# Performance work log

Measured on AMD Instinct MI355X. Metric: run time of the kernel, lower is better.

The kernel has to match this reference:

```python
import jax, jax.numpy as jnp
import numpy as np

BETA = 0.5

def gelu(x):
    return jax.nn.gelu(x, approximate=False)  # torch F.gelu default is exact erf

def setup_inputs() -> dict:
    key = jax.random.key(0)
    ks = jax.random.split(key, 10)
    N, F, PH, P, D, H, C, E = 50000, 128, 64, 8, 4, 128, 10, 1600000
    s = 0.05
    return {
        "x": jax.random.normal(ks[0], (N, F), jnp.float32),
        "W_proj": jax.random.normal(ks[1], (PH, F), jnp.float32) * s,
        "b_proj": jnp.zeros((PH,), jnp.float32),
        "W_x": jax.random.normal(ks[2], (H, F), jnp.float32) * s,
        "b_x": jnp.zeros((H,), jnp.float32),
        "W_path": jax.random.normal(ks[3], (H, D * PH), jnp.float32) * s,
        "b_path": jnp.zeros((H,), jnp.float32),
        "W_A": jax.random.normal(ks[4], (H, N), jnp.float32) * s,
        "b_A": jnp.zeros((H,), jnp.float32),
        "W_end": jax.random.normal(ks[5], (C, H), jnp.float32) * s,
        "b_end": jnp.zeros((C,), jnp.float32),
        "index": jax.random.randint(ks[6], (N, P, D), 0, N, jnp.int64)
                 if jax.config.jax_enable_x64 else jax.random.randint(ks[6], (N, P, D), 0, N, jnp.int32),
        "edge_index": jax.random.randint(ks[7], (2, E), 0, N, jnp.int32),
    }

def reference(x, W_proj, b_proj, W_x, b_x, W_path, b_path, W_A, b_A, W_end, b_end, index, edge_index):
    N = x.shape[0]
    # path projection then per-node path gather: [N, P, D, PH]
    pp = x @ W_proj.T + b_proj
    path = pp[index]
    Np, P, D, PH = path.shape
    # node MLP (dropout off in eval)
    h = gelu(x @ W_x.T + b_x)  # [N, H]
    # concat path encoder: [N, P, D*PH] -> [N, P, H]
    pi = gelu(path.reshape(Np, P, D * PH) @ W_path.T + b_path)
    # dot-product path attention with softmax over path dim
    att = jax.nn.softmax(jnp.einsum('nh,nph->np', h, pi), axis=-1)
    path_agg = jnp.einsum('np,nph->nh', att, pi)
    # sparse adjacency (COO, weights=1) times Linear weight: A @ W_A.T + b_A
    M = W_A.T  # [N, H]
    A_x = jax.ops.segment_sum(M[edge_index[1]], edge_index[0], num_segments=N) + b_A
    out = (1.0 - BETA) * (path_agg + h) + BETA * A_x
    out = gelu(out)
    return out @ W_end.T + b_end
```

## Files before the change

kernel.cpp:

```cpp
#include <hip/hip_runtime.h>
#include <hip/hip_bf16.h>
#include <math.h>

#define NF   128
#define NPH  64
#define NP   8
#define ND   4
#define NH   128
#define NC   10

typedef __bf16 bf16;
typedef __attribute__((ext_vector_type(4))) __bf16 bf16x4;
typedef __attribute__((ext_vector_type(8))) __bf16 bf16x8;
typedef __attribute__((ext_vector_type(4))) float f32x4;

__device__ __forceinline__ float gelu_fast(float x) {
    float z = fabsf(x) * 0.70710678118654752f;
    float t = 1.0f / (1.0f + 0.47047f * z);
    float poly = t * (0.3480242f + t * (-0.0958798f + t * 0.7478556f));
    float erfv = 1.0f - poly * __expf(-z * z);
    float s = copysignf(erfv, x);
    return 0.5f * x * (1.0f + s);
}

#define GLOAD_LDS16(g, l)                                                     \
    __builtin_amdgcn_global_load_lds(                                         \
        (const __attribute__((address_space(1))) unsigned int*)(g),           \
        (__attribute__((address_space(3))) unsigned int*)(l), 16, 0, 0)

__device__ __forceinline__ bf16x8 cvt8(float4 a, float4 b) {
    bf16x8 r;
    r[0] = (bf16)a.x; r[1] = (bf16)a.y; r[2] = (bf16)a.z; r[3] = (bf16)a.w;
    r[4] = (bf16)b.x; r[5] = (bf16)b.y; r[6] = (bf16)b.z; r[7] = (bf16)b.w;
    return r;
}

__global__ __launch_bounds__(256) void k_proj(
    const float* __restrict__ x,
    const float* __restrict__ Wproj, const float* __restrict__ bproj,
    const float* __restrict__ Wx,    const float* __restrict__ bx,
    bf16* __restrict__ pp, float* __restrict__ h, int N)
{
    __shared__ alignas(16) bf16 x_s[64 * 136];
    const int tid = threadIdx.x;
    const int w = tid >> 6, l = tid & 63;
    const int c = l & 15, g = l >> 4;

    bf16x8 bfr[3][4];
    float bias[3];
    #pragma unroll
    for (int t = 0; t < 3; ++t) {
        int ch = (w * 3 + t) * 16 + c;
        const float* wr = (ch < NPH) ? &Wproj[(size_t)ch * NF]
                                     : &Wx[(size_t)(ch - NPH) * NF];
        bias[t] = (ch < NPH) ? bproj[ch] : bx[ch - NPH];
        #pragma unroll
        for (int ks = 0; ks < 4; ++ks) {
            const float* src = wr + ks * 32 + g * 8;
            bfr[t][ks] = cvt8(*(const float4*)src, *(const float4*)(src + 4));
        }
    }

    const int n0 = blockIdx.x * 64;
    #pragma unroll
    for (int rr = 0; rr < 8; ++rr) {
        int id  = rr * 256 + tid;
        int row = id >> 5, c4 = id & 31;
        float4 v = make_float4(0.f, 0.f, 0.f, 0.f);
        if (n0 + row < N) v = *(const float4*)&x[(size_t)(n0 + row) * NF + c4 * 4];
        bf16x4 o;
        o[0] = (bf16)v.x; o[1] = (bf16)v.y; o[2] = (bf16)v.z; o[3] = (bf16)v.w;
        *(bf16x4*)&x_s[row * 136 + c4 * 4] = o;
    }
    __syncthreads();

    f32x4 acc[4][3] = {};
    #pragma unroll
    for (int rt = 0; rt < 4; ++rt)
        #pragma unroll
        for (int ks = 0; ks < 4; ++ks) {
            bf16x8 a = *(const bf16x8*)&x_s[(rt * 16 + c) * 136 + ks * 32 + g * 8];
            #pragma unroll
            for (int t = 0; t < 3; ++t)
                acc[rt][t] = __builtin_amdgcn_mfma_f32_16x16x32_bf16(
                    a, bfr[t][ks], acc[rt][t], 0, 0, 0);
        }

    #pragma unroll
    for (int rt = 0; rt < 4; ++rt) {
        #pragma unroll
        for (int t = 0; t < 3; ++t) {
            int ch = (w * 3 + t) * 16 + c;
            #pragma unroll
            for (int i = 0; i < 4; ++i) {
                int n = n0 + rt * 16 + g * 4 + i;
                if (n >= N) continue;
                float v = acc[rt][t][i] + bias[t];
                if (ch < NPH) pp[(size_t)n * NPH + ch] = (bf16)v;
                else          h[(size_t)n * NH + (ch - NPH)] = gelu_fast(v);
            }
        }
    }
}

__global__ __launch_bounds__(256) void k_path(
    const bf16* __restrict__ pp, const float* __restrict__ h,
    const float* __restrict__ Wpath, const float* __restrict__ bpath,
    const int* __restrict__ index, float* __restrict__ aggbuf,
    int N, int nrounds)
{
    __shared__ alignas(16) bf16 path_s[2][32 * 256];
    __shared__ alignas(16) float h_s[2][4][128];
    __shared__ float s_red[4][32];

    const int tid = threadIdx.x;
    const int w   = tid >> 6;
    const int l   = tid & 63;
    const int c   = l & 15;
    const int g   = l >> 4;
    const int nl  = g >> 1;
    const bool hi_half = (g & 1);

    bf16x8 bfrag[2][8];
    #pragma unroll
    for (int ht = 0; ht < 2; ++ht) {
        int hg = (w * 2 + ht) * 16 + c;
        #pragma unroll
        for (int ks = 0; ks < 8; ++ks) {
            const float* src = &Wpath[(size_t)hg * 256 + ks * 32 + g * 8];
            bfrag[ht][ks] = cvt8(*(const float4*)src, *(const float4*)(src + 4));
        }
    }
    const float bp0 = bpath[(w * 2 + 0) * 16 + c];
    const float bp1 = bpath[(w * 2 + 1) * 16 + c];

    auto stage = [&](int round, int b) {
        const int n0 = round * 4;
        #pragma unroll
        for (int rr = 0; rr < 4; ++rr) {
            int id  = rr * 256 + tid;
            int row = id >> 5;
            int cc  = id & 31;
            int ls  = cc ^ (row & 7);
            int d   = ls >> 3, q = ls & 7;
            int nn  = row >> 3, p = row & 7;
            int idx = index[(size_t)(n0 + nn) * (NP * ND) + p * ND + d];
            GLOAD_LDS16(pp + (size_t)idx * NPH + q * 8, &path_s[b][id * 8]);
        }
        if (tid < 128) {
            int node = tid >> 5, q = tid & 31;
            GLOAD_LDS16(&h[(size_t)(n0 + node) * NH + q * 4], &h_s[b][node][q * 4]);
        }
    };

    int r = blockIdx.x;
    const int G = gridDim.x;
    if (r < nrounds) stage(r, 0);
    int buf = 0;

    for (; r < nrounds; r += G) {
        const int n0 = r * 4;
        __syncthreads();
        if (r + G < nrounds) stage(r + G, buf ^ 1);

        f32x4 acc[2][2] = {};
        #pragma unroll
        for (int rt = 0; rt < 2; ++rt) {
            const int rowbase = (rt * 16 + c) * 256;
            #pragma unroll
            for (int ks = 0; ks < 8; ++ks) {
                int chunk = (ks * 4 + g) ^ (c & 7);
                bf16x8 a = *(const bf16x8*)&path_s[buf][rowbase + chunk * 8];
                acc[rt][0] = __builtin_amdgcn_mfma_f32_16x16x32_bf16(
                    a, bfrag[0][ks], acc[rt][0], 0, 0, 0);
                acc[rt][1] = __builtin_amdgcn_mfma_f32_16x16x32_bf16(
                    a, bfrag[1][ks], acc[rt][1], 0, 0, 0);
            }
        }

        float pi[2][2][4];
        #pragma unroll
        for (int rt = 0; rt < 2; ++rt) {
            const float hv0 = h_s[buf][rt * 2 + nl][w * 32 + c];
            const float hv1 = h_s[buf][rt * 2 + nl][w * 32 + 16 + c];
            float sp[4];
            #pragma unroll
            for (int i = 0; i < 4; ++i) {
                pi[rt][0][i] = gelu_fast(acc[rt][0][i] + bp0);
                pi[rt][1][i] = gelu_fast(acc[rt][1][i] + bp1);
                sp[i] = hv0 * pi[rt][0][i] + hv1 * pi[rt][1][i];
            }
            #pragma unroll
            for (int off = 1; off < 16; off <<= 1)
                #pragma unroll
                for (int i = 0; i < 4; ++i) sp[i] += __shfl_xor(sp[i], off, 64);
            float v = (c == 0) ? sp[0] : (c == 1) ? sp[1] : (c == 2) ? sp[2] : sp[3];
            if (c < 4) s_red[w][rt * 16 + g * 4 + c] = v;
        }

        __builtin_amdgcn_sched_barrier(0);
        asm volatile("s_waitcnt lgkmcnt(0)" ::: "memory");
        __builtin_amdgcn_s_barrier();
        __builtin_amdgcn_sched_barrier(0);

        #pragma unroll
        for (int rt = 0; rt < 2; ++rt) {
            float st[4];
            #pragma unroll
            for (int i = 0; i < 4; ++i) {
                int row = rt * 16 + g * 4 + i;
                st[i] = s_red[0][row] + s_red[1][row] +
                        s_red[2][row] + s_red[3][row];
            }
            float m4 = fmaxf(fmaxf(st[0], st[1]), fmaxf(st[2], st[3]));
            float m  = fmaxf(m4, __shfl_xor(m4, 16, 64));
            float e[4], s4 = 0.f;
            #pragma unroll
            for (int i = 0; i < 4; ++i) { e[i] = __expf(st[i] - m); s4 += e[i]; }
            float den = s4 + __shfl_xor(s4, 16, 64);
            const float inv = 1.0f / den;

            float pa0 = 0.f, pa1 = 0.f;
            #pragma unroll
            for (int i = 0; i < 4; ++i) {
                pa0 += e[i] * pi[rt][0][i];
                pa1 += e[i] * pi[rt][1][i];
            }
            pa0 = (pa0 + __shfl_xor(pa0, 16, 64)) * inv;
            pa1 = (pa1 + __shfl_xor(pa1, 16, 64)) * inv;

            if (!hi_half) {
                int n = n0 + rt * 2 + nl;
                const float hv0 = h_s[buf][rt * 2 + nl][w * 32 + c];
                const float hv1 = h_s[buf][rt * 2 + nl][w * 32 + 16 + c];
                aggbuf[(size_t)n * NH + w * 32 + c]      = 0.5f * (pa0 + hv0);
                aggbuf[(size_t)n * NH + w * 32 + 16 + c] = 0.5f * (pa1 + hv1);
            }
        }
        buf ^= 1;
    }
}

__global__ __launch_bounds__(256) void k_bhist(
    const int* __restrict__ esrc, int* __restrict__ bcnt, int E, int nbuck)
{
    __shared__ int hist[256];
    hist[threadIdx.x] = 0;
    __syncthreads();
    for (int i = blockIdx.x * 256 + threadIdx.x; i < E; i += gridDim.x * 256)
        atomicAdd(&hist[esrc[i] >> 8], 1);
    __syncthreads();
    if (threadIdx.x < nbuck && hist[threadIdx.x])
        atomicAdd(&bcnt[threadIdx.x], hist[threadIdx.x]);
}

__global__ __launch_bounds__(256) void k_bscan(
    const int* __restrict__ bcnt, int* __restrict__ gbase,
    int* __restrict__ gcur, int nbuck, int E)
{
    __shared__ int s[256];
    const int t = threadIdx.x;
    int v = (t < nbuck) ? bcnt[t] : 0;
    s[t] = v;
    __syncthreads();
    for (int off = 1; off < 256; off <<= 1) {
        int u = (t >= off) ? s[t - off] : 0;
        __syncthreads();
        s[t] += u;
        __syncthreads();
    }
    int ex = s[t] - v;
    if (t < nbuck) { gbase[t] = ex; gcur[t] = ex; }
    if (t == nbuck) gbase[t] = E;
}

__global__ __launch_bounds__(256) void k_bucket(
    const int* __restrict__ esrc, const int* __restrict__ edst,
    int* __restrict__ gcur, uint2* __restrict__ pairs, int E, int nbuck)
{
    __shared__ int cnt[256];
    __shared__ int bofs[256];
    const int tid = threadIdx.x;
    cnt[tid] = 0;
    __syncthreads();

    const int e0 = blockIdx.x * 2048;
    int src[8], dst[8], rk[8];
    #pragma unroll
    for (int k = 0; k < 8; ++k) {
        int i = e0 + k * 256 + tid;
        if (i < E) {
            src[k] = esrc[i]; dst[k] = edst[i];
            rk[k]  = atomicAdd(&cnt[src[k] >> 8], 1);
        } else src[k] = -1;
    }
    __syncthreads();
    if (tid < nbuck) {
        int cc = cnt[tid];
        bofs[tid] = cc ? atomicAdd(&gcur[tid], cc) : 0;
    }
    __syncthreads();
    #pragma unroll
    for (int k = 0; k < 8; ++k)
        if (src[k] >= 0)
            pairs[bofs[src[k] >> 8] + rk[k]] =
                make_uint2((unsigned)src[k], (unsigned)dst[k]);
}

__global__ __launch_bounds__(256) void k_bsort(
    const uint2* __restrict__ pairs, const int* __restrict__ gbase,
    int* __restrict__ sdst, int* __restrict__ base, int N, int E)
{
    __shared__ int hist[256], sc[256], cur[256];
    const int b = blockIdx.x, t = threadIdx.x;
    const int lo = gbase[b], hi = gbase[b + 1];
    hist[t] = 0;
    __syncthreads();
    for (int j = lo + t; j < hi; j += 256)
        atomicAdd(&hist[pairs[j].x & 255], 1);
    __syncthreads();
    int v = hist[t];
    sc[t] = v;
    __syncthreads();
    for (int off = 1; off < 256; off <<= 1) {
        int u = (t >= off) ? sc[t - off] : 0;
        __syncthreads();
        sc[t] += u;
        __syncthreads();
    }
    int ex = lo + sc[t] - v;
    cur[t] = ex;
    int n = b * 256 + t;
    if (n < N) base[n] = ex;
    if (b == 0 && t == 0) base[N] = E;
    __syncthreads();
    for (int j = lo + t; j < hi; j += 256) {
        uint2 p = pairs[j];
        int pos = atomicAdd(&cur[p.x & 255], 1);
        sdst[pos] = (int)p.y;
    }
}

__global__ __launch_bounds__(256) void k_transpose(
    const float* __restrict__ WA, bf16* __restrict__ M, int N)
{
    __shared__ float t[128][65];
    const int n0  = blockIdx.x * 64;
    const int tid = threadIdx.x;
    const int w = tid >> 6, l = tid & 63;
    #pragma unroll
    for (int rep = 0; rep < 32; ++rep) {
        int hh = rep * 4 + w;
        int n  = n0 + l;
        t[hh][l] = (n < N) ? WA[(size_t)hh * N + n] : 0.f;
    }
    __syncthreads();
    #pragma unroll
    for (int rep = 0; rep < 32; ++rep) {
        int n_l = rep * 2 + (tid >> 7);
        int n   = n0 + n_l;
        if (n < N) M[(size_t)n * NH + (tid & 127)] = (bf16)t[tid & 127][n_l];
    }
}

__device__ __forceinline__ void add8(float* a, uint4 v) {
    a[0] += __uint_as_float(v.x << 16);  a[1] += __uint_as_float(v.x & 0xffff0000u);
    a[2] += __uint_as_float(v.y << 16);  a[3] += __uint_as_float(v.y & 0xffff0000u);
    a[4] += __uint_as_float(v.z << 16);  a[5] += __uint_as_float(v.z & 0xffff0000u);
    a[6] += __uint_as_float(v.w << 16);  a[7] += __uint_as_float(v.w & 0xffff0000u);
}

__global__ __launch_bounds__(256) void k_spmm_out(
    const bf16* __restrict__ Mb, const int* __restrict__ base,
    const int* __restrict__ sdst, const float* __restrict__ aggbuf,
    const float* __restrict__ bA, const float* __restrict__ Wend,
    const float* __restrict__ bend, float* __restrict__ out, int N)
{
    __shared__ float wend_s[NC][128];
    __shared__ float bend_s[NC];
    const int tid = threadIdx.x;
    for (int id = tid; id < NC * 128; id += 256) wend_s[id >> 7][id & 127] = Wend[id];
    if (tid < NC) bend_s[tid] = bend[tid];
    __syncthreads();

    const int w = tid >> 6, l = tid & 63;
    const int n = blockIdx.x * 4 + w;
    if (n >= N) return;
    const int e = l >> 4, q = l & 15;
    const unsigned short* Mu = (const unsigned short*)Mb;

    const int b0 = base[n], b1 = base[n + 1];
    float acc[8] = {0.f, 0.f, 0.f, 0.f, 0.f, 0.f, 0.f, 0.f};
    int j = b0;
    for (; j + 16 <= b1; j += 16) {
        int d0 = sdst[j + e];
        int d1 = sdst[j + 4 + e];
        int d2 = sdst[j + 8 + e];
        int d3 = sdst[j + 12 + e];
        uint4 v0 = *((const uint4*)(Mu + (size_t)d0 * NH) + q);
        uint4 v1 = *((const uint4*)(Mu + (size_t)d1 * NH) + q);
        uint4 v2 = *((const uint4*)(Mu + (size_t)d2 * NH) + q);
        uint4 v3 = *((const uint4*)(Mu + (size_t)d3 * NH) + q);
        add8(acc, v0); add8(acc, v1); add8(acc, v2); add8(acc, v3);
    }
    for (; j + 4 <= b1; j += 4) {
        int d0 = sdst[j + e];
        uint4 v0 = *((const uint4*)(Mu + (size_t)d0 * NH) + q);
        add8(acc, v0);
    }
    if (e < b1 - j) {
        int d0 = sdst[j + e];
        uint4 v0 = *((const uint4*)(Mu + (size_t)d0 * NH) + q);
        add8(acc, v0);
    }
    #pragma unroll
    for (int k = 0; k < 8; ++k) {
        acc[k] += __shfl_xor(acc[k], 16, 64);
        acc[k] += __shfl_xor(acc[k], 32, 64);
    }

    float4 agA = *(const float4*)&aggbuf[(size_t)n * NH + q * 8];
    float4 agB = *(const float4*)&aggbuf[(size_t)n * NH + q * 8 + 4];
    float4 bA0 = *(const float4*)&bA[q * 8];
    float4 bA1 = *(const float4*)&bA[q * 8 + 4];
    float gg[8];
    gg[0] = gelu_fast(agA.x + 0.5f * (acc[0] + bA0.x));
    gg[1] = gelu_fast(agA.y + 0.5f * (acc[1] + bA0.y));
    gg[2] = gelu_fast(agA.z + 0.5f * (acc[2] + bA0.z));
    gg[3] = gelu_fast(agA.w + 0.5f * (acc[3] + bA0.w));
    gg[4] = gelu_fast(agB.x + 0.5f * (acc[4] + bA1.x));
    gg[5] = gelu_fast(agB.y + 0.5f * (acc[5] + bA1.y));
    gg[6] = gelu_fast(agB.z + 0.5f * (acc[6] + bA1.z));
    gg[7] = gelu_fast(agB.w + 0.5f * (acc[7] + bA1.w));

    float part[NC];
    #pragma unroll
    for (int cc = 0; cc < NC; ++cc) {
        float p = 0.f;
        #pragma unroll
        for (int k = 0; k < 8; ++k) p += gg[k] * wend_s[cc][q * 8 + k];
        part[cc] = p;
    }
    #pragma unroll
    for (int off = 1; off < 16; off <<= 1)
        #pragma unroll
        for (int cc = 0; cc < NC; ++cc) part[cc] += __shfl_xor(part[cc], off, 64);

    float r = part[0];
    #pragma unroll
    for (int cc = 1; cc < NC; ++cc) r = (l == cc) ? part[cc] : r;
    if (l < NC) out[(size_t)n * NC + l] = r + bend_s[l];
}

extern "C" void kernel_launch(void* const* d_in, const int* in_sizes, int n_in,
                              void* d_out, int out_size, void* d_ws, size_t ws_size,
                              hipStream_t stream)
{
    const float* x     = (const float*)d_in[0];
    const float* Wproj = (const float*)d_in[1];
    const float* bproj = (const float*)d_in[2];
    const float* Wx    = (const float*)d_in[3];
    const float* bx    = (const float*)d_in[4];
    const float* Wpath = (const float*)d_in[5];
    const float* bpath = (const float*)d_in[6];
    const float* WA    = (const float*)d_in[7];
    const float* bA    = (const float*)d_in[8];
    const float* Wend  = (const float*)d_in[9];
    const float* bend  = (const float*)d_in[10];
    const int*   index = (const int*)d_in[11];
    const int*   eidx  = (const int*)d_in[12];

    const int N = in_sizes[0] / NF;
    const int E = in_sizes[12] / 2;
    const int* esrc = eidx;
    const int* edst = eidx + E;
    const int nbuck = (N + 255) >> 8;

    char* p = (char*)d_ws;
    auto alloc = [&](size_t bytes) {
        char* r = p;
        p += (bytes + 255) & ~(size_t)255;
        return r;
    };
    bf16*  pp     = (bf16*)alloc((size_t)N * NPH * sizeof(bf16));
    float* h      = (float*)alloc((size_t)N * NH * sizeof(float));
    float* aggbuf = (float*)alloc((size_t)N * NH * sizeof(float));
    bf16*  Mb     = (bf16*)alloc((size_t)N * NH * sizeof(bf16));
    int*   base   = (int*)alloc((size_t)(N + 1) * sizeof(int));
    int*   sdst   = (int*)alloc((size_t)E * sizeof(int));
    int*   bcnt   = (int*)alloc(256 * sizeof(int));
    int*   gbase  = (int*)alloc(257 * sizeof(int));
    int*   gcur   = (int*)alloc(256 * sizeof(int));
    uint2* pairs  = (uint2*)alloc((size_t)E * sizeof(uint2));

    hipMemsetAsync(bcnt, 0, 256 * sizeof(int), stream);
    k_bhist<<<256, 256, 0, stream>>>(esrc, bcnt, E, nbuck);
    k_bscan<<<1, 256, 0, stream>>>(bcnt, gbase, gcur, nbuck, E);
    k_bucket<<<(E + 2047) / 2048, 256, 0, stream>>>(esrc, edst, gcur, pairs, E, nbuck);
    k_bsort<<<nbuck, 256, 0, stream>>>(pairs, gbase, sdst, base, N, E);
    k_transpose<<<(N + 63) / 64, 256, 0, stream>>>(WA, Mb, N);
    k_proj<<<(N + 63) / 64, 256, 0, stream>>>(x, Wproj, bproj, Wx, bx, pp, h, N);
    const int nrounds = N / 4;
    k_path<<<1024, 256, 0, stream>>>(pp, h, Wpath, bpath, index, aggbuf, N, nrounds);
    k_spmm_out<<<(N + 3) / 4, 256, 0, stream>>>(Mb, base, sdst, aggbuf, bA, Wend, bend,
                                                (float*)d_out, N);
}
```

Measured before the change: 286.7 us.

## Halve k_path per-round tile to two nodes and deepen spmm gather unroll

The path kernel now handles two nodes per round instead of four. This halves LDS staging and accumulator registers, precomputes the staging offsets, and raises launch bounds to 5 waves per SIMD with twice as many blocks, aiming for higher occupancy to hide gather latency. The spmm kernel adds a 32-edge unrolled loop so more independent gathers are in flight. The cost is more loop iterations and barriers per node in k_path and higher register pressure in the spmm loop.

```diff
diff --git a/kernel.cpp b/kernel.cpp
--- a/kernel.cpp
+++ b/kernel.cpp
@@ -103,15 +103,15 @@
     }
 }
 
-__global__ __launch_bounds__(256) void k_path(
+__global__ __launch_bounds__(256, 5) void k_path(
     const bf16* __restrict__ pp, const float* __restrict__ h,
     const float* __restrict__ Wpath, const float* __restrict__ bpath,
     const int* __restrict__ index, float* __restrict__ aggbuf,
     int N, int nrounds)
 {
-    __shared__ alignas(16) bf16 path_s[2][32 * 256];
-    __shared__ alignas(16) float h_s[2][4][128];
-    __shared__ float s_red[4][32];
+    __shared__ alignas(16) bf16 path_s[2][16 * 256];
+    __shared__ alignas(16) float h_s[2][2][128];
+    __shared__ float s_red[4][16];
 
     const int tid = threadIdx.x;
     const int w   = tid >> 6;
@@ -119,7 +119,15 @@
     const int c   = l & 15;
     const int g   = l >> 4;
     const int nl  = g >> 1;
-    const bool hi_half = (g & 1);
+
+    const int id0 = tid,        id1 = 256 + tid;
+    const int row0 = id0 >> 5,  row1 = id1 >> 5;
+    const int ls0 = (id0 & 31) ^ (row0 & 7);
+    const int ls1 = (id1 & 31) ^ (row1 & 7);
+    const int io0 = (row0 >> 3) * (NP * ND) + (row0 & 7) * ND + (ls0 >> 3);
+    const int io1 = (row1 >> 3) * (NP * ND) + (row1 & 7) * ND + (ls1 >> 3);
+    const int so0 = (ls0 & 7) * 8, so1 = (ls1 & 7) * 8;
+    const int lo0 = id0 * 8,       lo1 = id1 * 8;
 
     bf16x8 bfrag[2][8];
     #pragma unroll
@@ -135,22 +143,15 @@
     const float bp1 = bpath[(w * 2 + 1) * 16 + c];
 
     auto stage = [&](int round, int b) {
-        const int n0 = round * 4;
-        #pragma unroll
-        for (int rr = 0; rr < 4; ++rr) {
-            int id  = rr * 256 + tid;
-            int row = id >> 5;
-            int cc  = id & 31;
-            int ls  = cc ^ (row & 7);
-            int d   = ls >> 3, q = ls & 7;
-            int nn  = row >> 3, p = row & 7;
-            int idx = index[(size_t)(n0 + nn) * (NP * ND) + p * ND + d];
-            GLOAD_LDS16(pp + (size_t)idx * NPH + q * 8, &path_s[b][id * 8]);
-        }
-        if (tid < 128) {
-            int node = tid >> 5, q = tid & 31;
-            GLOAD_LDS16(&h[(size_t)(n0 + node) * NH + q * 4], &h_s[b][node][q * 4]);
-        }
+        const int n0 = round * 2;
+        const int* ib = index + (size_t)n0 * (NP * ND);
+        int idx0 = ib[io0];
+        int idx1 = ib[io1];
+        GLOAD_LDS16(pp + (size_t)idx0 * NPH + so0, &path_s[b][lo0]);
+        GLOAD_LDS16(pp + (size_t)idx1 * NPH + so1, &path_s[b][lo1]);
+        if (tid < 64)
+            GLOAD_LDS16(&h[(size_t)(n0 + (tid >> 5)) * NH + (tid & 31) * 4],
+                        &h_s[b][tid >> 5][(tid & 31) * 4]);
     };
 
     int r = blockIdx.x;
@@ -159,83 +160,69 @@
     int buf = 0;
 
     for (; r < nrounds; r += G) {
-        const int n0 = r * 4;
+        const int n0 = r * 2;
         __syncthreads();
         if (r + G < nrounds) stage(r + G, buf ^ 1);
 
-        f32x4 acc[2][2] = {};
-        #pragma unroll
-        for (int rt = 0; rt < 2; ++rt) {
-            const int rowbase = (rt * 16 + c) * 256;
+        f32x4 acc0 = {0.f, 0.f, 0.f, 0.f};
+        f32x4 acc1 = {0.f, 0.f, 0.f, 0.f};
+        const int rowbase = c * 256;
+        #pragma unroll
+        for (int ks = 0; ks < 8; ++ks) {
+            int chunk = (ks * 4 + g) ^ (c & 7);
+            bf16x8 a = *(const bf16x8*)&path_s[buf][rowbase + chunk * 8];
+            acc0 = __builtin_amdgcn_mfma_f32_16x16x32_bf16(a, bfrag[0][ks], acc0, 0, 0, 0);
+            acc1 = __builtin_amdgcn_mfma_f32_16x16x32_bf16(a, bfrag[1][ks], acc1, 0, 0, 0);
+        }
+
+        const float hv0 = h_s[buf][nl][w * 32 + c];
+        const float hv1 = h_s[buf][nl][w * 32 + 16 + c];
+        float pi0[4], pi1[4], sp[4];
+        #pragma unroll
+        for (int i = 0; i < 4; ++i) {
+            pi0[i] = gelu_fast(acc0[i] + bp0);
+            pi1[i] = gelu_fast(acc1[i] + bp1);
+            sp[i]  = hv0 * pi0[i] + hv1 * pi1[i];
+        }
+        #pragma unroll
+        for (int off = 1; off < 16; off <<= 1)
             #pragma unroll
-            for (int ks = 0; ks < 8; ++ks) {
-                int chunk = (ks * 4 + g) ^ (c & 7);
-                bf16x8 a = *(const bf16x8*)&path_s[buf][rowbase + chunk * 8];
-                acc[rt][0] = __builtin_amdgcn_mfma_f32_16x16x32_bf16(
-                    a, bfrag[0][ks], acc[rt][0], 0, 0, 0);
-                acc[rt][1] = __builtin_amdgcn_mfma_f32_16x16x32_bf16(
-                    a, bfrag[1][ks], acc[rt][1], 0, 0, 0);
-            }
-        }
-
-        float pi[2][2][4];
-        #pragma unroll
-        for (int rt = 0; rt < 2; ++rt) {
-            const float hv0 = h_s[buf][rt * 2 + nl][w * 32 + c];
-            const float hv1 = h_s[buf][rt * 2 + nl][w * 32 + 16 + c];
-            float sp[4];
-            #pragma unroll
-            for (int i = 0; i < 4; ++i) {
-                pi[rt][0][i] = gelu_fast(acc[rt][0][i] + bp0);
-                pi[rt][1][i] = gelu_fast(acc[rt][1][i] + bp1);
-                sp[i] = hv0 * pi[rt][0][i] + hv1 * pi[rt][1][i];
-            }
-            #pragma unroll
-            for (int off = 1; off < 16; off <<= 1)
-                #pragma unroll
-                for (int i = 0; i < 4; ++i) sp[i] += __shfl_xor(sp[i], off, 64);
-            float v = (c == 0) ? sp[0] : (c == 1) ? sp[1] : (c == 2) ? sp[2] : sp[3];
-            if (c < 4) s_red[w][rt * 16 + g * 4 + c] = v;
-        }
+            for (int i = 0; i < 4; ++i) sp[i] += __shfl_xor(sp[i], off, 64);
+        float v = (c == 0) ? sp[0] : (c == 1) ? sp[1] : (c == 2) ? sp[2] : sp[3];
+        if (c < 4) s_red[w][g * 4 + c] = v;
 
         __builtin_amdgcn_sched_barrier(0);
         asm volatile("s_waitcnt lgkmcnt(0)" ::: "memory");
         __builtin_amdgcn_s_barrier();
         __builtin_amdgcn_sched_barrier(0);
 
-        #pragma unroll
-        for (int rt = 0; rt < 2; ++rt) {
-            float st[4];
-            #pragma unroll
-            for (int i = 0; i < 4; ++i) {
-                int row = rt * 16 + g * 4 + i;
-                st[i] = s_red[0][row] + s_red[1][row] +
-                        s_red[2][row] + s_red[3][row];
-            }
-            float m4 = fmaxf(fmaxf(st[0], st[1]), fmaxf(st[2], st[3]));
-            float m  = fmaxf(m4, __shfl_xor(m4, 16, 64));
-            float e[4], s4 = 0.f;
-            #pragma unroll
-            for (int i = 0; i < 4; ++i) { e[i] = __expf(st[i] - m); s4 += e[i]; }
-            float den = s4 + __shfl_xor(s4, 16, 64);
-            const float inv = 1.0f / den;
-
-            float pa0 = 0.f, pa1 = 0.f;
-            #pragma unroll
-            for (int i = 0; i < 4; ++i) {
-                pa0 += e[i] * pi[rt][0][i];
-                pa1 += e[i] * pi[rt][1][i];
-            }
-            pa0 = (pa0 + __shfl_xor(pa0, 16, 64)) * inv;
-            pa1 = (pa1 + __shfl_xor(pa1, 16, 64)) * inv;
-
-            if (!hi_half) {
-                int n = n0 + rt * 2 + nl;
-                const float hv0 = h_s[buf][rt * 2 + nl][w * 32 + c];
-                const float hv1 = h_s[buf][rt * 2 + nl][w * 32 + 16 + c];
-                aggbuf[(size_t)n * NH + w * 32 + c]      = 0.5f * (pa0 + hv0);
-                aggbuf[(size_t)n * NH + w * 32 + 16 + c] = 0.5f * (pa1 + hv1);
-            }
+        float st[4];
+        #pragma unroll
+        for (int i = 0; i < 4; ++i) {
+            int row = g * 4 + i;
+            st[i] = s_red[0][row] + s_red[1][row] + s_red[2][row] + s_red[3][row];
+        }
+        float m4 = fmaxf(fmaxf(st[0], st[1]), fmaxf(st[2], st[3]));
+        float m  = fmaxf(m4, __shfl_xor(m4, 16, 64));
+        float e[4], s4 = 0.f;
+        #pragma unroll
+        for (int i = 0; i < 4; ++i) { e[i] = __expf(st[i] - m); s4 += e[i]; }
+        float den = s4 + __shfl_xor(s4, 16, 64);
+        const float inv = 1.0f / den;
+
+        float pa0 = 0.f, pa1 = 0.f;
+        #pragma unroll
+        for (int i = 0; i < 4; ++i) {
+            pa0 += e[i] * pi0[i];
+            pa1 += e[i] * pi1[i];
+        }
+        pa0 = (pa0 + __shfl_xor(pa0, 16, 64)) * inv;
+        pa1 = (pa1 + __shfl_xor(pa1, 16, 64)) * inv;
+
+        if (!(g & 1)) {
+            int n = n0 + nl;
+            aggbuf[(size_t)n * NH + w * 32 + c]      = 0.5f * (pa0 + hv0);
+            aggbuf[(size_t)n * NH + w * 32 + 16 + c] = 0.5f * (pa1 + hv1);
         }
         buf ^= 1;
     }
@@ -392,16 +379,27 @@
     const int b0 = base[n], b1 = base[n + 1];
     float acc[8] = {0.f, 0.f, 0.f, 0.f, 0.f, 0.f, 0.f, 0.f};
     int j = b0;
+    for (; j + 32 <= b1; j += 32) {
+        int d[8];
+        #pragma unroll
+        for (int k = 0; k < 8; ++k) d[k] = sdst[j + k * 4 + e];
+        uint4 v[8];
+        #pragma unroll
+        for (int k = 0; k < 8; ++k)
+            v[k] = *((const uint4*)(Mu + (size_t)d[k] * NH) + q);
+        #pragma unroll
+        for (int k = 0; k < 8; ++k) add8(acc, v[k]);
+    }
     for (; j + 16 <= b1; j += 16) {
-        int d0 = sdst[j + e];
-        int d1 = sdst[j + 4 + e];
-        int d2 = sdst[j + 8 + e];
-        int d3 = sdst[j + 12 + e];
-        uint4 v0 = *((const uint4*)(Mu + (size_t)d0 * NH) + q);
-        uint4 v1 = *((const uint4*)(Mu + (size_t)d1 * NH) + q);
-        uint4 v2 = *((const uint4*)(Mu + (size_t)d2 * NH) + q);
-        uint4 v3 = *((const uint4*)(Mu + (size_t)d3 * NH) + q);
-        add8(acc, v0); add8(acc, v1); add8(acc, v2); add8(acc, v3);
+        int d[4];
+        #pragma unroll
+        for (int k = 0; k < 4; ++k) d[k] = sdst[j + k * 4 + e];
+        uint4 v[4];
+        #pragma unroll
+        for (int k = 0; k < 4; ++k)
+            v[k] = *((const uint4*)(Mu + (size_t)d[k] * NH) + q);
+        #pragma unroll
+        for (int k = 0; k < 4; ++k) add8(acc, v[k]);
     }
     for (; j + 4 <= b1; j += 4) {
         int d0 = sdst[j + e];
@@ -500,8 +498,8 @@
     k_bsort<<<nbuck, 256, 0, stream>>>(pairs, gbase, sdst, base, N, E);
     k_transpose<<<(N + 63) / 64, 256, 0, stream>>>(WA, Mb, N);
     k_proj<<<(N + 63) / 64, 256, 0, stream>>>(x, Wproj, bproj, Wx, bx, pp, h, N);
-    const int nrounds = N / 4;
-    k_path<<<1024, 256, 0, stream>>>(pp, h, Wpath, bpath, index, aggbuf, N, nrounds);
+    const int nrounds = N / 2;
+    k_path<<<2048, 256, 0, stream>>>(pp, h, Wpath, bpath, index, aggbuf, N, nrounds);
     k_spmm_out<<<(N + 3) / 4, 256, 0, stream>>>(Mb, base, sdst, aggbuf, bA, Wend, bend,
                                                 (float*)d_out, N);
 }
```

Measured after the change: 448.3 us. 1.56x slower.

## Merge independent kernels into block-range dispatch kernels and deepen SpMM gather unroll

Applied to the files above, without the earlier changes.

Combines the projection, W_A transpose and edge histogram kernels into one launch, with each block choosing its role from blockIdx. Likewise merges the per-bucket sort with the path-attention kernel so the two run concurrently on disjoint block ranges. This cuts launch count and lets small, underutilizing stages overlap with heavier ones. It also adds a 32-edge unrolled gather loop in the SpMM to keep more loads in flight. The cost is higher register and LDS pressure from the union of roles in each kernel, and block-scheduling order now affects how much the stages actually overlap.

```diff
diff --git a/kernel.cpp b/kernel.cpp
--- a/kernel.cpp
+++ b/kernel.cpp
@@ -35,223 +35,109 @@
     return r;
 }
 
-__global__ __launch_bounds__(256) void k_proj(
+#define NBH 256
+
+__global__ __launch_bounds__(256) void k_front(
     const float* __restrict__ x,
     const float* __restrict__ Wproj, const float* __restrict__ bproj,
     const float* __restrict__ Wx,    const float* __restrict__ bx,
-    bf16* __restrict__ pp, float* __restrict__ h, int N)
+    bf16* __restrict__ pp, float* __restrict__ h,
+    const float* __restrict__ WA, bf16* __restrict__ Mb,
+    const int* __restrict__ esrc, int* __restrict__ bcnt,
+    int N, int E, int nbuck, int nbP, int nbT)
 {
-    __shared__ alignas(16) bf16 x_s[64 * 136];
+    __shared__ alignas(16) char smem[33280];
     const int tid = threadIdx.x;
-    const int w = tid >> 6, l = tid & 63;
-    const int c = l & 15, g = l >> 4;
-
-    bf16x8 bfr[3][4];
-    float bias[3];
-    #pragma unroll
-    for (int t = 0; t < 3; ++t) {
-        int ch = (w * 3 + t) * 16 + c;
-        const float* wr = (ch < NPH) ? &Wproj[(size_t)ch * NF]
-                                     : &Wx[(size_t)(ch - NPH) * NF];
-        bias[t] = (ch < NPH) ? bproj[ch] : bx[ch - NPH];
-        #pragma unroll
-        for (int ks = 0; ks < 4; ++ks) {
-            const float* src = wr + ks * 32 + g * 8;
-            bfr[t][ks] = cvt8(*(const float4*)src, *(const float4*)(src + 4));
-        }
-    }
-
-    const int n0 = blockIdx.x * 64;
-    #pragma unroll
-    for (int rr = 0; rr < 8; ++rr) {
-        int id  = rr * 256 + tid;
-        int row = id >> 5, c4 = id & 31;
-        float4 v = make_float4(0.f, 0.f, 0.f, 0.f);
-        if (n0 + row < N) v = *(const float4*)&x[(size_t)(n0 + row) * NF + c4 * 4];
-        bf16x4 o;
-        o[0] = (bf16)v.x; o[1] = (bf16)v.y; o[2] = (bf16)v.z; o[3] = (bf16)v.w;
-        *(bf16x4*)&x_s[row * 136 + c4 * 4] = o;
-    }
-    __syncthreads();
-
-    f32x4 acc[4][3] = {};
-    #pragma unroll
-    for (int rt = 0; rt < 4; ++rt)
-        #pragma unroll
-        for (int ks = 0; ks < 4; ++ks) {
-            bf16x8 a = *(const bf16x8*)&x_s[(rt * 16 + c) * 136 + ks * 32 + g * 8];
-            #pragma unroll
-            for (int t = 0; t < 3; ++t)
-                acc[rt][t] = __builtin_amdgcn_mfma_f32_16x16x32_bf16(
-                    a, bfr[t][ks], acc[rt][t], 0, 0, 0);
-        }
-
-    #pragma unroll
-    for (int rt = 0; rt < 4; ++rt) {
+    const int bid = blockIdx.x;
+
+    if (bid < nbP) {
+        bf16* x_s = (bf16*)smem;
+        const int w = tid >> 6, l = tid & 63;
+        const int c = l & 15, g = l >> 4;
+
+        bf16x8 bfr[3][4];
+        float bias[3];
         #pragma unroll
         for (int t = 0; t < 3; ++t) {
             int ch = (w * 3 + t) * 16 + c;
-            #pragma unroll
-            for (int i = 0; i < 4; ++i) {
-                int n = n0 + rt * 16 + g * 4 + i;
-                if (n >= N) continue;
-                float v = acc[rt][t][i] + bias[t];
-                if (ch < NPH) pp[(size_t)n * NPH + ch] = (bf16)v;
-                else          h[(size_t)n * NH + (ch - NPH)] = gelu_fast(v);
-            }
-        }
-    }
-}
-
-__global__ __launch_bounds__(256) void k_path(
-    const bf16* __restrict__ pp, const float* __restrict__ h,
-    const float* __restrict__ Wpath, const float* __restrict__ bpath,
-    const int* __restrict__ index, float* __restrict__ aggbuf,
-    int N, int nrounds)
-{
-    __shared__ alignas(16) bf16 path_s[2][32 * 256];
-    __shared__ alignas(16) float h_s[2][4][128];
-    __shared__ float s_red[4][32];
-
-    const int tid = threadIdx.x;
-    const int w   = tid >> 6;
-    const int l   = tid & 63;
-    const int c   = l & 15;
-    const int g   = l >> 4;
-    const int nl  = g >> 1;
-    const bool hi_half = (g & 1);
-
-    bf16x8 bfrag[2][8];
-    #pragma unroll
-    for (int ht = 0; ht < 2; ++ht) {
-        int hg = (w * 2 + ht) * 16 + c;
-        #pragma unroll
-        for (int ks = 0; ks < 8; ++ks) {
-            const float* src = &Wpath[(size_t)hg * 256 + ks * 32 + g * 8];
-            bfrag[ht][ks] = cvt8(*(const float4*)src, *(const float4*)(src + 4));
-        }
-    }
-    const float bp0 = bpath[(w * 2 + 0) * 16 + c];
-    const float bp1 = bpath[(w * 2 + 1) * 16 + c];
-
-    auto stage = [&](int round, int b) {
-        const int n0 = round * 4;
-        #pragma unroll
-        for (int rr = 0; rr < 4; ++rr) {
+            const float* wr = (ch < NPH) ? &Wproj[(size_t)ch * NF]
+                                         : &Wx[(size_t)(ch - NPH) * NF];
+            bias[t] = (ch < NPH) ? bproj[ch] : bx[ch - NPH];
+            #pragma unroll
+            for (int ks = 0; ks < 4; ++ks) {
+                const float* src = wr + ks * 32 + g * 8;
+                bfr[t][ks] = cvt8(*(const float4*)src, *(const float4*)(src + 4));
+            }
+        }
+
+        const int n0 = bid * 64;
+        #pragma unroll
+        for (int rr = 0; rr < 8; ++rr) {
             int id  = rr * 256 + tid;
-            int row = id >> 5;
-            int cc  = id & 31;
-            int ls  = cc ^ (row & 7);
-            int d   = ls >> 3, q = ls & 7;
-            int nn  = row >> 3, p = row & 7;
-            int idx = index[(size_t)(n0 + nn) * (NP * ND) + p * ND + d];
-            GLOAD_LDS16(pp + (size_t)idx * NPH + q * 8, &path_s[b][id * 8]);
-        }
-        if (tid < 128) {
-            int node = tid >> 5, q = tid & 31;
-            GLOAD_LDS16(&h[(size_t)(n0 + node) * NH + q * 4], &h_s[b][node][q * 4]);
-        }
-    };
-
-    int r = blockIdx.x;
-    const int G = gridDim.x;
-    if (r < nrounds) stage(r, 0);
-    int buf = 0;
-
-    for (; r < nrounds; r += G) {
-        const int n0 = r * 4;
-        __syncthreads();
-        if (r + G < nrounds) stage(r + G, buf ^ 1);
-
-        f32x4 acc[2][2] = {};
-        #pragma unroll
-        for (int rt = 0; rt < 2; ++rt) {
-            const int rowbase = (rt * 16 + c) * 256;
-            #pragma unroll
-            for (int ks = 0; ks < 8; ++ks) {
-                int chunk = (ks * 4 + g) ^ (c & 7);
-                bf16x8 a = *(const bf16x8*)&path_s[buf][rowbase + chunk * 8];
-                acc[rt][0] = __builtin_amdgcn_mfma_f32_16x16x32_bf16(
-                    a, bfrag[0][ks], acc[rt][0], 0, 0, 0);
-                acc[rt][1] = __builtin_amdgcn_mfma_f32_16x16x32_bf16(
-                    a, bfrag[1][ks], acc[rt][1], 0, 0, 0);
-            }
-        }
-
-        float pi[2][2][4];
-        #pragma unroll
-        for (int rt = 0; rt < 2; ++rt) {
-            const float hv0 = h_s[buf][rt * 2 + nl][w * 32 + c];
-            const float hv1 = h_s[buf][rt * 2 + nl][w * 32 + 16 + c];
-            float sp[4];
-            #pragma unroll
-            for (int i = 0; i < 4; ++i) {
-                pi[rt][0][i] = gelu_fast(acc[rt][0][i] + bp0);
-                pi[rt][1][i] = gelu_fast(acc[rt][1][i] + bp1);
-                sp[i] = hv0 * pi[rt][0][i] + hv1 * pi[rt][1][i];
-            }
-            #pragma unroll
-            for (int off = 1; off < 16; off <<= 1)
+            int row = id >> 5, c4 = id & 31;
+            float4 v = make_float4(0.f, 0.f, 0.f, 0.f);
+            if (n0 + row < N) v = *(const float4*)&x[(size_t)(n0 + row) * NF + c4 * 4];
+            bf16x4 o;
+            o[0] = (bf16)v.x; o[1] = (bf16)v.y; o[2] = (bf16)v.z; o[3] = (bf16)v.w;
+            *(bf16x4*)&x_s[row * 136 + c4 * 4] = o;
+        }
+        __syncthreads();
+
+        f32x4 acc[4][3] = {};
+        #pragma unroll
+        for (int rt = 0; rt < 4; ++rt)
+            #pragma unroll
+            for (int ks = 0; ks < 4; ++ks) {
+                bf16x8 a = *(const bf16x8*)&x_s[(rt * 16 + c) * 136 + ks * 32 + g * 8];
                 #pragma unroll
-                for (int i = 0; i < 4; ++i) sp[i] += __shfl_xor(sp[i], off, 64);
-            float v = (c == 0) ? sp[0] : (c == 1) ? sp[1] : (c == 2) ? sp[2] : sp[3];
-            if (c < 4) s_red[w][rt * 16 + g * 4 + c] = v;
-        }
-
-        __builtin_amdgcn_sched_barrier(0);
-        asm volatile("s_waitcnt lgkmcnt(0)" ::: "memory");
-        __builtin_amdgcn_s_barrier();
-        __builtin_amdgcn_sched_barrier(0);
-
-        #pragma unroll
-        for (int rt = 0; rt < 2; ++rt) {
-            float st[4];
-            #pragma unroll
-            for (int i = 0; i < 4; ++i) {
-                int row = rt * 16 + g * 4 + i;
-                st[i] = s_red[0][row] + s_red[1][row] +
-                        s_red[2][row] + s_red[3][row];
-            }
-            float m4 = fmaxf(fmaxf(st[0], st[1]), fmaxf(st[2], st[3]));
-            float m  = fmaxf(m4, __shfl_xor(m4, 16, 64));
-            float e[4], s4 = 0.f;
-            #pragma unroll
-            for (int i = 0; i < 4; ++i) { e[i] = __expf(st[i] - m); s4 += e[i]; }
-            float den = s4 + __shfl_xor(s4, 16, 64);
-            const float inv = 1.0f / den;
-
-            float pa0 = 0.f, pa1 = 0.f;
-            #pragma unroll
-            for (int i = 0; i < 4; ++i) {
-                pa0 += e[i] * pi[rt][0][i];
-                pa1 += e[i] * pi[rt][1][i];
-            }
-            pa0 = (pa0 + __shfl_xor(pa0, 16, 64)) * inv;
-            pa1 = (pa1 + __shfl_xor(pa1, 16, 64)) * inv;
-
-            if (!hi_half) {
-                int n = n0 + rt * 2 + nl;
-                const float hv0 = h_s[buf][rt * 2 + nl][w * 32 + c];
-                const float hv1 = h_s[buf][rt * 2 + nl][w * 32 + 16 + c];
-                aggbuf[(size_t)n * NH + w * 32 + c]      = 0.5f * (pa0 + hv0);
-                aggbuf[(size_t)n * NH + w * 32 + 16 + c] = 0.5f * (pa1 + hv1);
-            }
-        }
-        buf ^= 1;
-    }
-}
-
-__global__ __launch_bounds__(256) void k_bhist(
-    const int* __restrict__ esrc, int* __restrict__ bcnt, int E, int nbuck)
-{
-    __shared__ int hist[256];
-    hist[threadIdx.x] = 0;
-    __syncthreads();
-    for (int i = blockIdx.x * 256 + threadIdx.x; i < E; i += gridDim.x * 256)
-        atomicAdd(&hist[esrc[i] >> 8], 1);
-    __syncthreads();
-    if (threadIdx.x < nbuck && hist[threadIdx.x])
-        atomicAdd(&bcnt[threadIdx.x], hist[threadIdx.x]);
+                for (int t = 0; t < 3; ++t)
+                    acc[rt][t] = __builtin_amdgcn_mfma_f32_16x16x32_bf16(
+                        a, bfr[t][ks], acc[rt][t], 0, 0, 0);
+            }
+
+        #pragma unroll
+        for (int rt = 0; rt < 4; ++rt) {
+            #pragma unroll
+            for (int t = 0; t < 3; ++t) {
+                int ch = (w * 3 + t) * 16 + c;
+                #pragma unroll
+                for (int i = 0; i < 4; ++i) {
+                    int n = n0 + rt * 16 + g * 4 + i;
+                    if (n >= N) continue;
+                    float v = acc[rt][t][i] + bias[t];
+                    if (ch < NPH) pp[(size_t)n * NPH + ch] = (bf16)v;
+                    else          h[(size_t)n * NH + (ch - NPH)] = gelu_fast(v);
+                }
+            }
+        }
+    } else if (bid < nbP + nbT) {
+        float* tt = (float*)smem;
+        const int n0 = (bid - nbP) * 64;
+        const int w = tid >> 6, l = tid & 63;
+        #pragma unroll
+        for (int rep = 0; rep < 32; ++rep) {
+            int hh = rep * 4 + w;
+            int n  = n0 + l;
+            tt[hh * 65 + l] = (n < N) ? WA[(size_t)hh * N + n] : 0.f;
+        }
+        __syncthreads();
+        #pragma unroll
+        for (int rep = 0; rep < 32; ++rep) {
+            int n_l = rep * 2 + (tid >> 7);
+            int n   = n0 + n_l;
+            if (n < N) Mb[(size_t)n * NH + (tid & 127)] = (bf16)tt[(tid & 127) * 65 + n_l];
+        }
+    } else {
+        int* hist = (int*)smem;
+        hist[tid] = 0;
+        __syncthreads();
+        const int hb = bid - nbP - nbT;
+        for (int i = hb * 256 + tid; i < E; i += NBH * 256)
+            atomicAdd(&hist[esrc[i] >> 8], 1);
+        __syncthreads();
+        if (tid < nbuck && hist[tid])
+            atomicAdd(&bcnt[tid], hist[tid]);
+    }
 }
 
 __global__ __launch_bounds__(256) void k_bscan(
@@ -307,59 +193,179 @@
                 make_uint2((unsigned)src[k], (unsigned)dst[k]);
 }
 
-__global__ __launch_bounds__(256) void k_bsort(
+__global__ __launch_bounds__(256) void k_mid(
     const uint2* __restrict__ pairs, const int* __restrict__ gbase,
-    int* __restrict__ sdst, int* __restrict__ base, int N, int E)
+    int* __restrict__ sdst, int* __restrict__ base,
+    const bf16* __restrict__ pp, const float* __restrict__ h,
+    const float* __restrict__ Wpath, const float* __restrict__ bpath,
+    const int* __restrict__ index, float* __restrict__ aggbuf,
+    int N, int E, int nbuck, int nrounds)
 {
-    __shared__ int hist[256], sc[256], cur[256];
-    const int b = blockIdx.x, t = threadIdx.x;
-    const int lo = gbase[b], hi = gbase[b + 1];
-    hist[t] = 0;
-    __syncthreads();
-    for (int j = lo + t; j < hi; j += 256)
-        atomicAdd(&hist[pairs[j].x & 255], 1);
-    __syncthreads();
-    int v = hist[t];
-    sc[t] = v;
-    __syncthreads();
-    for (int off = 1; off < 256; off <<= 1) {
-        int u = (t >= off) ? sc[t - off] : 0;
-        __syncthreads();
-        sc[t] += u;
-        __syncthreads();
-    }
-    int ex = lo + sc[t] - v;
-    cur[t] = ex;
-    int n = b * 256 + t;
-    if (n < N) base[n] = ex;
-    if (b == 0 && t == 0) base[N] = E;
-    __syncthreads();
-    for (int j = lo + t; j < hi; j += 256) {
-        uint2 p = pairs[j];
-        int pos = atomicAdd(&cur[p.x & 255], 1);
-        sdst[pos] = (int)p.y;
-    }
-}
-
-__global__ __launch_bounds__(256) void k_transpose(
-    const float* __restrict__ WA, bf16* __restrict__ M, int N)
-{
-    __shared__ float t[128][65];
-    const int n0  = blockIdx.x * 64;
+    __shared__ alignas(16) char smem[37376];
     const int tid = threadIdx.x;
-    const int w = tid >> 6, l = tid & 63;
-    #pragma unroll
-    for (int rep = 0; rep < 32; ++rep) {
-        int hh = rep * 4 + w;
-        int n  = n0 + l;
-        t[hh][l] = (n < N) ? WA[(size_t)hh * N + n] : 0.f;
-    }
-    __syncthreads();
-    #pragma unroll
-    for (int rep = 0; rep < 32; ++rep) {
-        int n_l = rep * 2 + (tid >> 7);
-        int n   = n0 + n_l;
-        if (n < N) M[(size_t)n * NH + (tid & 127)] = (bf16)t[tid & 127][n_l];
+
+    if (blockIdx.x < nbuck) {
+        int* hist = (int*)smem;
+        int* sc   = hist + 256;
+        int* cur  = hist + 512;
+        const int b = blockIdx.x, t = tid;
+        const int lo = gbase[b], hi = gbase[b + 1];
+        hist[t] = 0;
+        __syncthreads();
+        for (int j = lo + t; j < hi; j += 256)
+            atomicAdd(&hist[pairs[j].x & 255], 1);
+        __syncthreads();
+        int v = hist[t];
+        sc[t] = v;
+        __syncthreads();
+        for (int off = 1; off < 256; off <<= 1) {
+            int u = (t >= off) ? sc[t - off] : 0;
+            __syncthreads();
+            sc[t] += u;
+            __syncthreads();
+        }
+        int ex = lo + sc[t] - v;
+        cur[t] = ex;
+        int n = b * 256 + t;
+        if (n < N) base[n] = ex;
+        if (b == 0 && t == 0) base[N] = E;
+        __syncthreads();
+        for (int j = lo + t; j < hi; j += 256) {
+            uint2 p = pairs[j];
+            int pos = atomicAdd(&cur[p.x & 255], 1);
+            sdst[pos] = (int)p.y;
+        }
+        return;
+    }
+
+    bf16*  path_s = (bf16*)smem;
+    float* h_sf   = (float*)(smem + 32768);
+    float* s_red  = (float*)(smem + 36864);
+
+    const int w   = tid >> 6;
+    const int l   = tid & 63;
+    const int c   = l & 15;
+    const int g   = l >> 4;
+    const int nl  = g >> 1;
+
+    bf16x8 bfrag[2][8];
+    #pragma unroll
+    for (int ht = 0; ht < 2; ++ht) {
+        int hg = (w * 2 + ht) * 16 + c;
+        #pragma unroll
+        for (int ks = 0; ks < 8; ++ks) {
+            const float* src = &Wpath[(size_t)hg * 256 + ks * 32 + g * 8];
+            bfrag[ht][ks] = cvt8(*(const float4*)src, *(const float4*)(src + 4));
+        }
+    }
+    const float bp0 = bpath[(w * 2 + 0) * 16 + c];
+    const float bp1 = bpath[(w * 2 + 1) * 16 + c];
+
+    auto stage = [&](int round, int b) {
+        const int n0 = round * 4;
+        #pragma unroll
+        for (int rr = 0; rr < 4; ++rr) {
+            int id  = rr * 256 + tid;
+            int row = id >> 5;
+            int cc  = id & 31;
+            int ls  = cc ^ (row & 7);
+            int d   = ls >> 3, q = ls & 7;
+            int nn  = row >> 3, p = row & 7;
+            int idx = index[(size_t)(n0 + nn) * (NP * ND) + p * ND + d];
+            GLOAD_LDS16(pp + (size_t)idx * NPH + q * 8, &path_s[b * 8192 + id * 8]);
+        }
+        if (tid < 128) {
+            int node = tid >> 5, q = tid & 31;
+            GLOAD_LDS16(&h[(size_t)(n0 + node) * NH + q * 4],
+                        &h_sf[(b * 4 + node) * 128 + q * 4]);
+        }
+    };
+
+    int r = blockIdx.x - nbuck;
+    const int G = gridDim.x - nbuck;
+    if (r < nrounds) stage(r, 0);
+    int buf = 0;
+
+    for (; r < nrounds; r += G) {
+        const int n0 = r * 4;
+        __syncthreads();
+        if (r + G < nrounds) stage(r + G, buf ^ 1);
+
+        f32x4 acc[2][2] = {};
+        #pragma unroll
+        for (int rt = 0; rt < 2; ++rt) {
+            const int rowbase = buf * 8192 + (rt * 16 + c) * 256;
+            #pragma unroll
+            for (int ks = 0; ks < 8; ++ks) {
+                int chunk = (ks * 4 + g) ^ (c & 7);
+                bf16x8 a = *(const bf16x8*)&path_s[rowbase + chunk * 8];
+                acc[rt][0] = __builtin_amdgcn_mfma_f32_16x16x32_bf16(
+                    a, bfrag[0][ks], acc[rt][0], 0, 0, 0);
+                acc[rt][1] = __builtin_amdgcn_mfma_f32_16x16x32_bf16(
+                    a, bfrag[1][ks], acc[rt][1], 0, 0, 0);
+            }
+        }
+
+        float pi[2][2][4];
+        #pragma unroll
+        for (int rt = 0; rt < 2; ++rt) {
+            const float hv0 = h_sf[(buf * 4 + rt * 2 + nl) * 128 + w * 32 + c];
+            const float hv1 = h_sf[(buf * 4 + rt * 2 + nl) * 128 + w * 32 + 16 + c];
+            float sp[4];
+            #pragma unroll
+            for (int i = 0; i < 4; ++i) {
+                pi[rt][0][i] = gelu_fast(acc[rt][0][i] + bp0);
+                pi[rt][1][i] = gelu_fast(acc[rt][1][i] + bp1);
+                sp[i] = hv0 * pi[rt][0][i] + hv1 * pi[rt][1][i];
+            }
+            #pragma unroll
+            for (int off = 1; off < 16; off <<= 1)
+                #pragma unroll
+                for (int i = 0; i < 4; ++i) sp[i] += __shfl_xor(sp[i], off, 64);
+            float v = (c == 0) ? sp[0] : (c == 1) ? sp[1] : (c == 2) ? sp[2] : sp[3];
+            if (c < 4) s_red[w * 32 + rt * 16 + g * 4 + c] = v;
+        }
+
+        __builtin_amdgcn_sched_barrier(0);
+        asm volatile("s_waitcnt lgkmcnt(0)" ::: "memory");
+        __builtin_amdgcn_s_barrier();
+        __builtin_amdgcn_sched_barrier(0);
+
+        #pragma unroll
+        for (int rt = 0; rt < 2; ++rt) {
+            float st[4];
+            #pragma unroll
+            for (int i = 0; i < 4; ++i) {
+                int row = rt * 16 + g * 4 + i;
+                st[i] = s_red[0 * 32 + row] + s_red[1 * 32 + row] +
+                        s_red[2 * 32 + row] + s_red[3 * 32 + row];
+            }
+            float m4 = fmaxf(fmaxf(st[0], st[1]), fmaxf(st[2], st[3]));
+            float m  = fmaxf(m4, __shfl_xor(m4, 16, 64));
+            float e[4], s4 = 0.f;
+            #pragma unroll
+            for (int i = 0; i < 4; ++i) { e[i] = __expf(st[i] - m); s4 += e[i]; }
+            float den = s4 + __shfl_xor(s4, 16, 64);
+            const float inv = 1.0f / den;
+
+            float pa0 = 0.f, pa1 = 0.f;
+            #pragma unroll
+            for (int i = 0; i < 4; ++i) {
+                pa0 += e[i] * pi[rt][0][i];
+                pa1 += e[i] * pi[rt][1][i];
+            }
+            pa0 = (pa0 + __shfl_xor(pa0, 16, 64)) * inv;
+            pa1 = (pa1 + __shfl_xor(pa1, 16, 64)) * inv;
+
+            if (!(g & 1)) {
+                int n = n0 + rt * 2 + nl;
+                const float hv0 = h_sf[(buf * 4 + rt * 2 + nl) * 128 + w * 32 + c];
+                const float hv1 = h_sf[(buf * 4 + rt * 2 + nl) * 128 + w * 32 + 16 + c];
+                aggbuf[(size_t)n * NH + w * 32 + c]      = 0.5f * (pa0 + hv0);
+                aggbuf[(size_t)n * NH + w * 32 + 16 + c] = 0.5f * (pa1 + hv1);
+            }
+        }
+        buf ^= 1;
     }
 }
 
@@ -392,16 +398,27 @@
     const int b0 = base[n], b1 = base[n + 1];
     float acc[8] = {0.f, 0.f, 0.f, 0.f, 0.f, 0.f, 0.f, 0.f};
     int j = b0;
+    for (; j + 32 <= b1; j += 32) {
+        int d[8];
+        #pragma unroll
+        for (int k = 0; k < 8; ++k) d[k] = sdst[j + k * 4 + e];
+        uint4 v[8];
+        #pragma unroll
+        for (int k = 0; k < 8; ++k)
+            v[k] = *((const uint4*)(Mu + (size_t)d[k] * NH) + q);
+        #pragma unroll
+        for (int k = 0; k < 8; ++k) add8(acc, v[k]);
+    }
     for (; j + 16 <= b1; j += 16) {
-        int d0 = sdst[j + e];
-        int d1 = sdst[j + 4 + e];
-        int d2 = sdst[j + 8 + e];
-        int d3 = sdst[j + 12 + e];
-        uint4 v0 = *((const uint4*)(Mu + (size_t)d0 * NH) + q);
-        uint4 v1 = *((const uint4*)(Mu + (size_t)d1 * NH) + q);
-        uint4 v2 = *((const uint4*)(Mu + (size_t)d2 * NH) + q);
-        uint4 v3 = *((const uint4*)(Mu + (size_t)d3 * NH) + q);
-        add8(acc, v0); add8(acc, v1); add8(acc, v2); add8(acc, v3);
+        int d[4];
+        #pragma unroll
+        for (int k = 0; k < 4; ++k) d[k] = sdst[j + k * 4 + e];
+        uint4 v[4];
+        #pragma unroll
+        for (int k = 0; k < 4; ++k)
+            v[k] = *((const uint4*)(Mu + (size_t)d[k] * NH) + q);
+        #pragma unroll
+        for (int k = 0; k < 4; ++k) add8(acc, v[k]);
     }
     for (; j + 4 <= b1; j += 4) {
         int d0 = sdst[j + e];
@@ -493,15 +510,19 @@
     int*   gcur   = (int*)alloc(256 * sizeof(int));
     uint2* pairs  = (uint2*)alloc((size_t)E * sizeof(uint2));
 
+    const int nbP = (N + 63) / 64;
+    const int nbT = (N + 63) / 64;
+    const int NPATH = 1024;
+    const int nrounds = N / 4;
+
     hipMemsetAsync(bcnt, 0, 256 * sizeof(int), stream);
-    k_bhist<<<256, 256, 0, stream>>>(esrc, bcnt, E, nbuck);
+    k_front<<<nbP + nbT + NBH, 256, 0, stream>>>(
+        x, Wproj, bproj, Wx, bx, pp, h, WA, Mb, esrc, bcnt, N, E, nbuck, nbP, nbT);
     k_bscan<<<1, 256, 0, stream>>>(bcnt, gbase, gcur, nbuck, E);
     k_bucket<<<(E + 2047) / 2048, 256, 0, stream>>>(esrc, edst, gcur, pairs, E, nbuck);
-    k_bsort<<<nbuck, 256, 0, stream>>>(pairs, gbase, sdst, base, N, E);
-    k_transpose<<<(N + 63) / 64, 256, 0, stream>>>(WA, Mb, N);
-    k_proj<<<(N + 63) / 64, 256, 0, stream>>>(x, Wproj, bproj, Wx, bx, pp, h, N);
-    const int nrounds = N / 4;
-    k_path<<<1024, 256, 0, stream>>>(pp, h, Wpath, bpath, index, aggbuf, N, nrounds);
+    k_mid<<<nbuck + NPATH, 256, 0, stream>>>(
+        pairs, gbase, sdst, base, pp, h, Wpath, bpath, index, aggbuf,
+        N, E, nbuck, nrounds);
     k_spmm_out<<<(N + 3) / 4, 256, 0, stream>>>(Mb, base, sdst, aggbuf, bA, Wend, bend,
                                                 (float*)d_out, N);
 }
```

New measurement: 273.2 us. 4.7% less time.
